# Performance work log

Hardware: AMD Instinct MI355X
Metric: run time of the kernel (lower is better)

## Reference

```python
import jax, jax.numpy as jnp
import numpy as np

EPS = 1e-10


def setup_inputs() -> dict:
    key = jax.random.key(0)
    k1, k2, k3, k4 = jax.random.split(key, 4)
    B, V, K, S = 8192, 32000, 5, 100  # batch, vocab, negatives per sample, sampling domain
    yHat = jax.random.normal(k1, (B, V), dtype=jnp.float32)
    raw = jax.random.uniform(k2, (V, S), dtype=jnp.float32, minval=0.1, maxval=1.0)
    prob = raw / raw.sum(axis=1, keepdims=True)  # row-stochastic sampling table [V,100]
    y = jax.random.randint(k3, (B,), 0, V)
    ind = jax.random.randint(k4, (B, K), 0, S)  # pre-drawn weighted-sample indices
    return {"yHat": yHat, "prob": prob, "y": y, "ind": ind}


def reference(yHat, prob, y, ind):
    # Stable shift: max is detached in the original (torch .detach())
    maxxx = jax.lax.stop_gradient(jnp.max(yHat, axis=-1, keepdims=True))
    yh = yHat - maxxx
    # Gather target logit [B,1] and k sampled negative logits [B,k]
    Yg = jnp.take_along_axis(yh, y[:, None], axis=1)
    comp = jnp.take_along_axis(yh, ind, axis=1)
    # Importance weights p = 1/prob[y][ind]  (prob is a constant table in torch)
    prow = prob[y]  # [B,100]
    p = 1.0 / jnp.take_along_axis(prow, ind, axis=1)  # [B,k]
    complement = p * jnp.exp(comp)
    q = jnp.min(p, axis=-1, keepdims=True)
    Yg = q * jnp.exp(Yg)
    out = jnp.concatenate([Yg, complement], axis=1)  # [B,k+1]
    out = out / jnp.sum(out, axis=1, keepdims=True)
    out_c = 1.0 - out
    k1 = out.shape[1]
    mask = jnp.zeros((1, k1), dtype=out.dtype).at[0, 0].set(1.0)
    loss = -(jnp.log(out + EPS) * mask + jnp.log(out_c + EPS) * (1.0 - mask)).mean()
    return loss
```

## Files before the change

### kernel.cpp

```cpp
#include <hip/hip_runtime.h>
#include <math.h>

#define B_ROWS 8192
#define V_COLS 32000
#define K_NEG  5
#define S_DOM  100
#define EPSF   1e-10f

__global__ __launch_bounds__(256) void blackout_row_kernel(
    const float* __restrict__ yHat,
    const float* __restrict__ prob,
    const int*   __restrict__ y,
    const int*   __restrict__ ind,
    float*       __restrict__ row_loss)
{
    const int r   = blockIdx.x;
    const int tid = threadIdx.x;
    const float* __restrict__ row = yHat + (size_t)r * V_COLS;

    const float4* __restrict__ row4 = (const float4*)row;
    float m = -INFINITY;
    #pragma unroll 4
    for (int i = tid; i < V_COLS / 4; i += 256) {
        float4 v = row4[i];
        m = fmaxf(m, fmaxf(fmaxf(v.x, v.y), fmaxf(v.z, v.w)));
    }
    #pragma unroll
    for (int off = 32; off > 0; off >>= 1)
        m = fmaxf(m, __shfl_down(m, off, 64));
    __shared__ float smax[4];
    if ((tid & 63) == 0) smax[tid >> 6] = m;
    __syncthreads();

    if (tid == 0) {
        const float mm = fmaxf(fmaxf(smax[0], smax[1]), fmaxf(smax[2], smax[3]));

        const int yy = y[r];
        const float* __restrict__ prow = prob + (size_t)yy * S_DOM;

        float p[K_NEG], comp[K_NEG];
        float q = INFINITY;
        #pragma unroll
        for (int j = 0; j < K_NEG; ++j) {
            const int ij = ind[r * K_NEG + j];
            const float pv = 1.0f / prow[ij];
            p[j] = pv;
            q = fminf(q, pv);
            comp[j] = row[ij] - mm;
        }
        const float Yg = row[yy] - mm;

        float v[K_NEG + 1];
        v[0] = q * expf(Yg);
        float sum = v[0];
        #pragma unroll
        for (int j = 0; j < K_NEG; ++j) {
            v[j + 1] = p[j] * expf(comp[j]);
            sum += v[j + 1];
        }
        const float inv_sum = 1.0f / sum;

        float lr = logf(v[0] * inv_sum + EPSF);
        #pragma unroll
        for (int j = 1; j <= K_NEG; ++j)
            lr += logf(1.0f - v[j] * inv_sum + EPSF);

        row_loss[r] = lr;
    }
}

__global__ __launch_bounds__(256) void blackout_reduce_kernel(
    const float* __restrict__ row_loss,
    float*       __restrict__ out)
{
    const int tid = threadIdx.x;
    float s = 0.0f;
    for (int i = tid; i < B_ROWS; i += 256)
        s += row_loss[i];
    #pragma unroll
    for (int off = 32; off > 0; off >>= 1)
        s += __shfl_down(s, off, 64);
    __shared__ float sh[4];
    if ((tid & 63) == 0) sh[tid >> 6] = s;
    __syncthreads();
    if (tid == 0) {
        const float tot = sh[0] + sh[1] + sh[2] + sh[3];
        out[0] = -tot / (float)(B_ROWS * (K_NEG + 1));
    }
}

extern "C" void kernel_launch(void* const* d_in, const int* in_sizes, int n_in,
                              void* d_out, int out_size, void* d_ws, size_t ws_size,
                              hipStream_t stream) {
    const float* yHat = (const float*)d_in[0];
    const float* prob = (const float*)d_in[1];
    const int*   y    = (const int*)d_in[2];
    const int*   ind  = (const int*)d_in[3];
    float* out = (float*)d_out;
    float* row_loss = (float*)d_ws;

    blackout_row_kernel<<<B_ROWS, 256, 0, stream>>>(yHat, prob, y, ind, row_loss);
    blackout_reduce_kernel<<<1, 256, 0, stream>>>(row_loss, out);
}
```

Baseline: 1.301 ms.

## Drop full-row max scan; use local max of gathered logits for stability

The softmax over the target and sampled logits is shift-invariant, so the per-row max over all vocabulary columns is replaced by the max of the six gathered values. Each thread now handles one row and only gathers a handful of elements instead of streaming the whole row. This removes nearly all global memory traffic, though rounding may differ slightly from the reference's global-max shift.

```diff
diff --git a/kernel.cpp b/kernel.cpp
--- a/kernel.cpp
+++ b/kernel.cpp
@@ -7,66 +7,53 @@
 #define S_DOM  100
 #define EPSF   1e-10f
 
-__global__ __launch_bounds__(256) void blackout_row_kernel(
+__global__ __launch_bounds__(256) void blackout_gather_kernel(
     const float* __restrict__ yHat,
     const float* __restrict__ prob,
     const int*   __restrict__ y,
     const int*   __restrict__ ind,
     float*       __restrict__ row_loss)
 {
-    const int r   = blockIdx.x;
-    const int tid = threadIdx.x;
-    const float* __restrict__ row = yHat + (size_t)r * V_COLS;
+    const int r = blockIdx.x * 256 + threadIdx.x;
+    if (r >= B_ROWS) return;
 
-    const float4* __restrict__ row4 = (const float4*)row;
-    float m = -INFINITY;
-    #pragma unroll 4
-    for (int i = tid; i < V_COLS / 4; i += 256) {
-        float4 v = row4[i];
-        m = fmaxf(m, fmaxf(fmaxf(v.x, v.y), fmaxf(v.z, v.w)));
+    const int yy = y[r];
+    const float* __restrict__ row  = yHat + (size_t)r  * V_COLS;
+    const float* __restrict__ prow = prob + (size_t)yy * S_DOM;
+
+    int ij[K_NEG];
+    #pragma unroll
+    for (int j = 0; j < K_NEG; ++j)
+        ij[j] = ind[r * K_NEG + j];
+
+    const float t = row[yy];
+    float p[K_NEG], c[K_NEG];
+    float q = INFINITY;
+    float m = t;
+    #pragma unroll
+    for (int j = 0; j < K_NEG; ++j) {
+        p[j] = 1.0f / prow[ij[j]];
+        q    = fminf(q, p[j]);
+        c[j] = row[ij[j]];
+        m    = fmaxf(m, c[j]);
     }
+
+    const float v0 = q * expf(t - m);
+    float sum = v0;
+    float v[K_NEG];
     #pragma unroll
-    for (int off = 32; off > 0; off >>= 1)
-        m = fmaxf(m, __shfl_down(m, off, 64));
-    __shared__ float smax[4];
-    if ((tid & 63) == 0) smax[tid >> 6] = m;
-    __syncthreads();
+    for (int j = 0; j < K_NEG; ++j) {
+        v[j] = p[j] * expf(c[j] - m);
+        sum += v[j];
+    }
+    const float inv_sum = 1.0f / sum;
 
-    if (tid == 0) {
-        const float mm = fmaxf(fmaxf(smax[0], smax[1]), fmaxf(smax[2], smax[3]));
+    float lr = logf(v0 * inv_sum + EPSF);
+    #pragma unroll
+    for (int j = 0; j < K_NEG; ++j)
+        lr += logf(1.0f - v[j] * inv_sum + EPSF);
 
-        const int yy = y[r];
-        const float* __restrict__ prow = prob + (size_t)yy * S_DOM;
-
-        float p[K_NEG], comp[K_NEG];
-        float q = INFINITY;
-        #pragma unroll
-        for (int j = 0; j < K_NEG; ++j) {
-            const int ij = ind[r * K_NEG + j];
-            const float pv = 1.0f / prow[ij];
-            p[j] = pv;
-            q = fminf(q, pv);
-            comp[j] = row[ij] - mm;
-        }
-        const float Yg = row[yy] - mm;
-
-        float v[K_NEG + 1];
-        v[0] = q * expf(Yg);
-        float sum = v[0];
-        #pragma unroll
-        for (int j = 0; j < K_NEG; ++j) {
-            v[j + 1] = p[j] * expf(comp[j]);
-            sum += v[j + 1];
-        }
-        const float inv_sum = 1.0f / sum;
-
-        float lr = logf(v[0] * inv_sum + EPSF);
-        #pragma unroll
-        for (int j = 1; j <= K_NEG; ++j)
-            lr += logf(1.0f - v[j] * inv_sum + EPSF);
-
-        row_loss[r] = lr;
-    }
+    row_loss[r] = lr;
 }
 
 __global__ __launch_bounds__(256) void blackout_reduce_kernel(
@@ -99,6 +86,6 @@
     float* out = (float*)d_out;
     float* row_loss = (float*)d_ws;
 
-    blackout_row_kernel<<<B_ROWS, 256, 0, stream>>>(yHat, prob, y, ind, row_loss);
+    blackout_gather_kernel<<<B_ROWS / 256, 256, 0, stream>>>(yHat, prob, y, ind, row_loss);
     blackout_reduce_kernel<<<1, 256, 0, stream>>>(row_loss, out);
 }
```

After: 1.106 ms. 1.18x faster.
